# Kernel optimization log

Hardware: AMD Instinct MI355X
Metric: run time of the kernel (lower is better)

The kernel has to match this reference:

```python
import jax, jax.numpy as jnp
import numpy as np

N, E, B = 200000, 800000, 16
NODE_FEAT = 140  # last col = shape element type id
N_OPS, N_TYPES = 120, 8
OP_EMB, TYPE_EMB, CFG = 32, 4, 18
H = 64
CAT = (NODE_FEAT - 1) + TYPE_EMB + OP_EMB + CFG  # 193


def _lin(k, i, o):
    s = 1.0 / np.sqrt(i)
    return jax.random.uniform(k, (i, o), jnp.float32, -s, s)


def setup_inputs() -> dict:
    key = jax.random.key(0)
    ks = jax.random.split(key, 20)
    nf = jax.random.normal(ks[0], (N, NODE_FEAT - 1), jnp.float32)
    ty = jax.random.randint(ks[1], (N, 1), 0, N_TYPES).astype(jnp.float32)
    inp = {
        "node_feat": jnp.concatenate([nf, ty], axis=1),
        "node_config_feat": jax.random.normal(ks[2], (N, CFG), jnp.float32),
        "node_opcode": jax.random.randint(ks[3], (N,), 0, N_OPS),
        "edge_index": jax.random.randint(ks[4], (2, E), 0, N),
        "batch": jnp.sort(jax.random.randint(ks[5], (N,), 0, B)),
        "op_emb": jax.random.normal(ks[6], (N_OPS, OP_EMB), jnp.float32),
        "type_emb": jax.random.normal(ks[7], (N_TYPES, TYPE_EMB), jnp.float32),
        "lin_w": _lin(ks[8], CAT, 2 * H),
        "lin_b": jnp.zeros((2 * H,), jnp.float32),
        "post_w": _lin(ks[9], H, 1),
        "post_b": jnp.zeros((1,), jnp.float32),
    }
    kk = 10
    for l, ind in enumerate([2 * H, H, H]):
        inp[f"p{l}_wp"] = _lin(ks[kk], ind, ind); kk += 1  # SAGE project lin
        inp[f"p{l}_bp"] = jnp.zeros((ind,), jnp.float32)
        inp[f"p{l}_wl"] = _lin(ks[kk], ind, H); kk += 1    # lin_l (on aggregated)
        inp[f"p{l}_bl"] = jnp.zeros((H,), jnp.float32)
        inp[f"p{l}_wr"] = _lin(ks[kk], ind, H); kk += 1    # lin_r (root, no bias)
    return inp


def _sage(x, src, dst, deg_inv, wp, bp, wl, bl, wr):
    # PyG SAGEConv(project=True, normalize=True), mean aggregation
    xp = jax.nn.relu(x @ wp + bp)
    agg = jax.ops.segment_sum(xp[src], dst, num_segments=x.shape[0]) * deg_inv
    out = agg @ wl + bl + x @ wr
    n = jnp.linalg.norm(out, axis=-1, keepdims=True)
    return out / jnp.maximum(n, 1e-12)


def reference(node_feat, node_config_feat, node_opcode, edge_index, batch,
              op_emb, type_emb, lin_w, lin_b, post_w, post_b,
              p0_wp, p0_bp, p0_wl, p0_bl, p0_wr,
              p1_wp, p1_bp, p1_wl, p1_bl, p1_wr,
              p2_wp, p2_bp, p2_wl, p2_bl, p2_wr):
    lps = [(p0_wp, p0_bp, p0_wl, p0_bl, p0_wr),
           (p1_wp, p1_bp, p1_wl, p1_bl, p1_wr),
           (p2_wp, p2_bp, p2_wl, p2_bl, p2_wr)]
    ty = jnp.take(type_emb, node_feat[:, -1].astype(jnp.int32), axis=0)
    op = jnp.take(op_emb, node_opcode, axis=0)
    x = jnp.concatenate([node_feat[:, :-1], ty, op, node_config_feat], axis=-1)
    x = jax.nn.relu(x @ lin_w + lin_b)  # (N, 128)
    src, dst = edge_index[0], edge_index[1]
    deg = jax.ops.segment_sum(jnp.ones((E,), x.dtype), dst, num_segments=N)
    deg_inv = (1.0 / jnp.maximum(deg, 1.0))[:, None]
    for (wp, bp, wl, bl, wr) in lps:
        x = _sage(x, src, dst, deg_inv, wp, bp, wl, bl, wr)
    # global max + mean pool per graph
    gmax = jax.ops.segment_max(x, batch, num_segments=B)
    gsum = jax.ops.segment_sum(x, batch, num_segments=B)
    cnt = jax.ops.segment_sum(jnp.ones((N,), x.dtype), batch, num_segments=B)
    g = gmax + gsum / jnp.maximum(cnt, 1.0)[:, None]
    g = g / jnp.linalg.norm(g, axis=-1, keepdims=True)
    return g @ post_w + post_b  # (B, 1); eval path returns x_graph
```

## Files before the change

### kernel.cpp

```cpp
#include <hip/hip_runtime.h>

typedef _Float16 half8 __attribute__((ext_vector_type(8)));
typedef _Float16 h4 __attribute__((ext_vector_type(4)));
typedef float f32x4 __attribute__((ext_vector_type(4)));

__device__ __forceinline__ unsigned fkey(float f) {
  unsigned u = __float_as_uint(f);
  return (u & 0x80000000u) ? ~u : (u | 0x80000000u);
}
__device__ __forceinline__ float funkey(unsigned k) {
  unsigned u = (k & 0x80000000u) ? (k ^ 0x80000000u) : ~k;
  return __uint_as_float(u);
}

struct WD { const float* src; _Float16* dst; int K, NC, Kpad, base; };
struct WDs { WD d[10]; int total; };

__global__ __launch_bounds__(256) void k_wconv(WDs w) {
  int idx = blockIdx.x * 256 + threadIdx.x;
  if (idx >= w.total) return;
#pragma unroll
  for (int i = 0; i < 10; ++i) {
    int rel = idx - w.d[i].base;
    int sz = w.d[i].NC * w.d[i].Kpad;
    if (rel >= 0 && rel < sz) {
      int n = rel / w.d[i].Kpad;
      int k = rel - n * w.d[i].Kpad;
      w.d[i].dst[rel] = (k < w.d[i].K) ? (_Float16)w.d[i].src[(size_t)k * w.d[i].NC + n]
                                       : (_Float16)0.f;
      return;
    }
  }
}

__global__ __launch_bounds__(256) void k_count(const int* __restrict__ dst,
                                               int* __restrict__ counts, int E) {
  int e = blockIdx.x * 256 + threadIdx.x;
  if (e < E) atomicAdd(&counts[dst[e]], 1);
}

__global__ __launch_bounds__(256) void k_scan1(const int* __restrict__ counts,
                                               int* __restrict__ offsets,
                                               int* __restrict__ blockSums, int N) {
  __shared__ int sm[256];
  int tid = threadIdx.x;
  int gid = blockIdx.x * 256 + tid;
  int v = (gid < N) ? counts[gid] : 0;
  sm[tid] = v;
  __syncthreads();
  for (int off = 1; off < 256; off <<= 1) {
    int t = (tid >= off) ? sm[tid - off] : 0;
    __syncthreads();
    sm[tid] += t;
    __syncthreads();
  }
  if (gid < N) offsets[gid] = sm[tid] - v;
  if (tid == 255) blockSums[blockIdx.x] = sm[255];
}

__global__ __launch_bounds__(1024) void k_scan2(int* __restrict__ blockSums, int NB) {
  __shared__ int sm[1024];
  int tid = threadIdx.x;
  int v = (tid < NB) ? blockSums[tid] : 0;
  sm[tid] = v;
  __syncthreads();
  for (int off = 1; off < 1024; off <<= 1) {
    int t = (tid >= off) ? sm[tid - off] : 0;
    __syncthreads();
    sm[tid] += t;
    __syncthreads();
  }
  if (tid < NB) blockSums[tid] = sm[tid] - v;
}

__global__ __launch_bounds__(256) void k_scan3(const int* __restrict__ counts,
                                               int* __restrict__ offsets,
                                               const int* __restrict__ blockSums,
                                               int* __restrict__ fillpos,
                                               float* __restrict__ deginv, int N, int E) {
  int gid = blockIdx.x * 256 + threadIdx.x;
  if (gid < N) {
    int off = offsets[gid] + blockSums[gid >> 8];
    offsets[gid] = off;
    fillpos[gid] = off;
    deginv[gid] = 1.f / fmaxf((float)counts[gid], 1.f);
  }
  if (gid == 0) offsets[N] = E;
}

__global__ __launch_bounds__(256) void k_fill(const int* __restrict__ src,
                                              const int* __restrict__ dst,
                                              int* __restrict__ fillpos,
                                              int* __restrict__ esrc, int E) {
  int e = blockIdx.x * 256 + threadIdx.x;
  if (e < E) {
    int p = atomicAdd(&fillpos[dst[e]], 1);
    esrc[p] = src[e];
  }
}

__global__ __launch_bounds__(256) void k_feat(const float* __restrict__ node_feat,
                                              const float* __restrict__ cfgf,
                                              const int* __restrict__ opcode,
                                              const float* __restrict__ op_emb,
                                              const float* __restrict__ type_emb,
                                              _Float16* __restrict__ Out, int N) {
  __shared__ _Float16 sM[64 * 96];
  const int base = blockIdx.x * 64;

#pragma unroll
  for (int it = 0; it < 5; ++it) {
    int t = it * 256 + threadIdx.x;
    if (t >= 1088) break;
    int r = t / 17, c = t - r * 17;
    int n = base + r;
    if (n < N) {
      const float4* g = (const float4*)(node_feat + (size_t)n * 140 + c * 8);
      float4 v0 = g[0], v1 = g[1];
      half8 o;
      o[0] = (_Float16)v0.x; o[1] = (_Float16)v0.y;
      o[2] = (_Float16)v0.z; o[3] = (_Float16)v0.w;
      o[4] = (_Float16)v1.x; o[5] = (_Float16)v1.y;
      o[6] = (_Float16)v1.z; o[7] = (_Float16)v1.w;
      *(half8*)(Out + (size_t)n * 224 + c * 8) = o;
    }
  }

  const int wave = threadIdx.x >> 6, lane = threadIdx.x & 63;
#pragma unroll
  for (int it = 0; it < 3; ++it) {
    int cls = it * 4 + wave;
    if (cls >= 11) break;
    int r = lane, n = base + r;
    bool ok = (n < N);
    half8 o = half8{};
    if (cls == 0) {
      if (ok) {
        float4 v = *(const float4*)(node_feat + (size_t)n * 140 + 136);
        int ty = min(max((int)v.w, 0), 7);
        const float* te = type_emb + ty * 4;
        o[0] = (_Float16)v.x; o[1] = (_Float16)v.y; o[2] = (_Float16)v.z;
        o[3] = (_Float16)te[0]; o[4] = (_Float16)te[1];
        o[5] = (_Float16)te[2]; o[6] = (_Float16)te[3];
        o[7] = (_Float16)op_emb[opcode[n] * 32];
      }
    } else if (cls <= 3) {
      if (ok) {
        const float* oe = op_emb + opcode[n] * 32 + ((cls - 1) * 8 + 1);
#pragma unroll
        for (int j = 0; j < 8; ++j) o[j] = (_Float16)oe[j];
      }
    } else if (cls == 4) {
      if (ok) {
        const float* oe = op_emb + opcode[n] * 32;
#pragma unroll
        for (int j = 0; j < 7; ++j) o[j] = (_Float16)oe[25 + j];
        o[7] = (_Float16)cfgf[(size_t)n * 18];
      }
    } else if (cls <= 6) {
      if (ok) {
        const float* cf = cfgf + (size_t)n * 18 + ((cls - 5) * 8 + 1);
#pragma unroll
        for (int j = 0; j < 8; ++j) o[j] = (_Float16)cf[j];
      }
    } else if (cls == 7) {
      if (ok) o[0] = (_Float16)cfgf[(size_t)n * 18 + 17];
    }
    *(half8*)(sM + r * 96 + cls * 8) = o;
  }
  __syncthreads();

#pragma unroll
  for (int it = 0; it < 3; ++it) {
    int t = it * 256 + threadIdx.x;
    if (t >= 704) break;
    int r = t / 11, cc = t - r * 11;
    int n = base + r;
    if (n < N)
      *(half8*)(Out + (size_t)n * 224 + 136 + cc * 8) = *(const half8*)(sM + r * 96 + cc * 8);
  }
}

template <int K0, int K1, int NC, int MODE>
__global__ __launch_bounds__(256) void k_mm(
    const _Float16* __restrict__ A0, const _Float16* __restrict__ W0,
    const _Float16* __restrict__ A1, const _Float16* __restrict__ W1,
    const float* __restrict__ bias, _Float16* __restrict__ Out, int N) {
  constexpr int NT = NC / 16;
  constexpr int RT = 4;
  constexpr int KP0 = K0 + 8;
  constexpr int KP1 = K1 + 8;
  __shared__ _Float16 sB0[NC * KP0];
  __shared__ _Float16 sB1[(K1 > 0) ? (NC * KP1) : 8];

  for (int idx = threadIdx.x; idx < NC * (K0 / 8); idx += 256) {
    int nn = idx / (K0 / 8), k8 = idx - nn * (K0 / 8);
    *(half8*)(sB0 + nn * KP0 + k8 * 8) = *(const half8*)(W0 + (size_t)nn * K0 + k8 * 8);
  }
  if constexpr (K1 > 0) {
    for (int idx = threadIdx.x; idx < NC * (K1 / 8); idx += 256) {
      int nn = idx / (K1 / 8), k8 = idx - nn * (K1 / 8);
      *(half8*)(sB1 + nn * KP1 + k8 * 8) = *(const half8*)(W1 + (size_t)nn * K1 + k8 * 8);
    }
  }
  __syncthreads();

  const int lane = threadIdx.x & 63, wave = threadIdx.x >> 6;
  const int quad = lane >> 4, l15 = lane & 15;
  const int r0 = blockIdx.x * 256 + wave * 64;

  f32x4 acc[RT][NT];
#pragma unroll
  for (int rt = 0; rt < RT; ++rt)
#pragma unroll
    for (int t = 0; t < NT; ++t) acc[rt][t] = (f32x4)0.f;

  {
    const _Float16* ap = A0 + (size_t)(r0 + l15) * K0 + quad * 8;
#pragma unroll
    for (int k = 0; k < K0; k += 32) {
      half8 a[RT];
#pragma unroll
      for (int rt = 0; rt < RT; ++rt) a[rt] = *(const half8*)(ap + (size_t)rt * 16 * K0 + k);
#pragma unroll
      for (int t = 0; t < NT; ++t) {
        half8 b = *(const half8*)(sB0 + (t * 16 + l15) * KP0 + quad * 8 + k);
#pragma unroll
        for (int rt = 0; rt < RT; ++rt)
          acc[rt][t] = __builtin_amdgcn_mfma_f32_16x16x32_f16(a[rt], b, acc[rt][t], 0, 0, 0);
      }
    }
  }
  if constexpr (K1 > 0) {
    const _Float16* ap = A1 + (size_t)(r0 + l15) * K1 + quad * 8;
#pragma unroll
    for (int k = 0; k < K1; k += 32) {
      half8 a[RT];
#pragma unroll
      for (int rt = 0; rt < RT; ++rt) a[rt] = *(const half8*)(ap + (size_t)rt * 16 * K1 + k);
#pragma unroll
      for (int t = 0; t < NT; ++t) {
        half8 b = *(const half8*)(sB1 + (t * 16 + l15) * KP1 + quad * 8 + k);
#pragma unroll
        for (int rt = 0; rt < RT; ++rt)
          acc[rt][t] = __builtin_amdgcn_mfma_f32_16x16x32_f16(a[rt], b, acc[rt][t], 0, 0, 0);
      }
    }
  }

#pragma unroll
  for (int rt = 0; rt < RT; ++rt) {
#pragma unroll
    for (int t = 0; t < NT; ++t) {
      float bv = bias[t * 16 + l15];
      acc[rt][t][0] += bv; acc[rt][t][1] += bv;
      acc[rt][t][2] += bv; acc[rt][t][3] += bv;
    }
    if constexpr (MODE == 1) {
      f32x4 ss = (f32x4)0.f;
#pragma unroll
      for (int t = 0; t < NT; ++t) ss += acc[rt][t] * acc[rt][t];
#pragma unroll
      for (int j = 0; j < 4; ++j) {
        float s = ss[j];
        s += __shfl_xor(s, 1);
        s += __shfl_xor(s, 2);
        s += __shfl_xor(s, 4);
        s += __shfl_xor(s, 8);
        float sc = 1.f / fmaxf(sqrtf(s), 1e-12f);
#pragma unroll
        for (int t = 0; t < NT; ++t) acc[rt][t][j] *= sc;
      }
    } else {
#pragma unroll
      for (int t = 0; t < NT; ++t) {
        acc[rt][t][0] = fmaxf(acc[rt][t][0], 0.f);
        acc[rt][t][1] = fmaxf(acc[rt][t][1], 0.f);
        acc[rt][t][2] = fmaxf(acc[rt][t][2], 0.f);
        acc[rt][t][3] = fmaxf(acc[rt][t][3], 0.f);
      }
    }
#pragma unroll
    for (int j = 0; j < 4; ++j) {
      int r = r0 + rt * 16 + quad * 4 + j;
      if (r < N) {
#pragma unroll
        for (int t = 0; t < NT; ++t)
          Out[(size_t)r * NC + t * 16 + l15] = (_Float16)acc[rt][t][j];
      }
    }
  }
}

template <int NC>
__global__ __launch_bounds__(256) void k_agg(const _Float16* __restrict__ xp,
                                             const int* __restrict__ offs,
                                             const int* __restrict__ esrc,
                                             const float* __restrict__ deginv,
                                             _Float16* __restrict__ agg, int N) {
  constexpr int LPN = NC / 4;
  int t = blockIdx.x * 256 + threadIdx.x;
  int node = t / LPN;
  int lane = t - node * LPN;
  if (node >= N) return;
  int s0 = offs[node], s1 = offs[node + 1];
  double a0 = 0., a1 = 0., a2 = 0., a3 = 0.;
  for (int i = s0; i < s1; i += 4) {
    int nlast = s1 - 1;
    int e0 = esrc[i];
    int e1 = esrc[min(i + 1, nlast)];
    int e2 = esrc[min(i + 2, nlast)];
    int e3 = esrc[min(i + 3, nlast)];
    h4 v0 = ((const h4*)(xp + (size_t)e0 * NC))[lane];
    h4 v1 = ((const h4*)(xp + (size_t)e1 * NC))[lane];
    h4 v2 = ((const h4*)(xp + (size_t)e2 * NC))[lane];
    h4 v3 = ((const h4*)(xp + (size_t)e3 * NC))[lane];
    a0 += (double)(float)v0[0]; a1 += (double)(float)v0[1];
    a2 += (double)(float)v0[2]; a3 += (double)(float)v0[3];
    if (i + 1 < s1) { a0 += (double)(float)v1[0]; a1 += (double)(float)v1[1];
                      a2 += (double)(float)v1[2]; a3 += (double)(float)v1[3]; }
    if (i + 2 < s1) { a0 += (double)(float)v2[0]; a1 += (double)(float)v2[1];
                      a2 += (double)(float)v2[2]; a3 += (double)(float)v2[3]; }
    if (i + 3 < s1) { a0 += (double)(float)v3[0]; a1 += (double)(float)v3[1];
                      a2 += (double)(float)v3[2]; a3 += (double)(float)v3[3]; }
  }
  double di = (double)deginv[node];
  h4 o;
  o[0] = (_Float16)(a0 * di); o[1] = (_Float16)(a1 * di);
  o[2] = (_Float16)(a2 * di); o[3] = (_Float16)(a3 * di);
  ((h4*)(agg + (size_t)node * NC))[lane] = o;
}

__global__ __launch_bounds__(256) void k_pool1(const _Float16* __restrict__ x,
                                               const int* __restrict__ batch,
                                               unsigned* __restrict__ gkey,
                                               double* __restrict__ gsum,
                                               int* __restrict__ gcnt, int N) {
  int chunk = blockIdx.x * 4 + (threadIdx.x >> 6);
  int lane = threadIdx.x & 63;
  int n0 = chunk * 64;
  if (n0 >= N) return;
  int n1 = min(n0 + 64, N);
  float rmax = -3.4e38f;
  double rsum = 0.;
  int rcnt = 0, curb = batch[n0];
  for (int n = n0; n < n1; ++n) {
    int b = batch[n];
    if (b != curb) {
      atomicMax(&gkey[curb * 64 + lane], fkey(rmax));
      atomicAdd(&gsum[curb * 64 + lane], rsum);
      if (lane == 0) atomicAdd(&gcnt[curb], rcnt);
      rmax = -3.4e38f; rsum = 0.; rcnt = 0; curb = b;
    }
    float v = (float)x[(size_t)n * 64 + lane];
    rmax = fmaxf(rmax, v);
    rsum += (double)v;
    rcnt++;
  }
  atomicMax(&gkey[curb * 64 + lane], fkey(rmax));
  atomicAdd(&gsum[curb * 64 + lane], rsum);
  if (lane == 0) atomicAdd(&gcnt[curb], rcnt);
}

__global__ __launch_bounds__(1024) void k_pool2(const unsigned* __restrict__ gkey,
                                                const double* __restrict__ gsum,
                                                const int* __restrict__ gcnt,
                                                const float* __restrict__ post_w,
                                                const float* __restrict__ post_b,
                                                float* __restrict__ out) {
  int b = threadIdx.x >> 6, lane = threadIdx.x & 63;
  float m = funkey(gkey[b * 64 + lane]);
  double s = gsum[b * 64 + lane];
  double c = (double)gcnt[b];
  float g = m + (float)(s / fmax(c, 1.0));
  float ss = g * g;
#pragma unroll
  for (int off = 1; off < 64; off <<= 1) ss += __shfl_xor(ss, off);
  float gn = g / fmaxf(sqrtf(ss), 1e-30f);
  float contrib = gn * post_w[lane];
#pragma unroll
  for (int off = 1; off < 64; off <<= 1) contrib += __shfl_xor(contrib, off);
  if (lane == 0) out[b] = contrib + post_b[0];
}

extern "C" void kernel_launch(void* const* d_in, const int* in_sizes, int n_in,
                              void* d_out, int out_size, void* d_ws, size_t ws_size,
                              hipStream_t stream) {
  const float* node_feat = (const float*)d_in[0];
  const float* cfgf      = (const float*)d_in[1];
  const int*   opcode    = (const int*)d_in[2];
  const int*   eidx      = (const int*)d_in[3];
  const int*   batch     = (const int*)d_in[4];
  const float* op_emb    = (const float*)d_in[5];
  const float* type_emb  = (const float*)d_in[6];
  const float* lin_w     = (const float*)d_in[7];
  const float* lin_b     = (const float*)d_in[8];
  const float* post_w    = (const float*)d_in[9];
  const float* post_b    = (const float*)d_in[10];
  const float* wp[3] = {(const float*)d_in[11], (const float*)d_in[16], (const float*)d_in[21]};
  const float* bp[3] = {(const float*)d_in[12], (const float*)d_in[17], (const float*)d_in[22]};
  const float* wl[3] = {(const float*)d_in[13], (const float*)d_in[18], (const float*)d_in[23]};
  const float* bl[3] = {(const float*)d_in[14], (const float*)d_in[19], (const float*)d_in[24]};
  const float* wr[3] = {(const float*)d_in[15], (const float*)d_in[20], (const float*)d_in[25]};

  const int N = in_sizes[2];
  const int E = in_sizes[3] / 2;
  const int NPAD = ((N + 255) / 256) * 256;
  const int* e_src = eidx;
  const int* e_dst = eidx + E;

  char* p = (char*)d_ws;
  auto alloc = [&](size_t bytes) -> void* {
    void* r = (void*)p;
    p += (bytes + 255) & ~(size_t)255;
    return r;
  };
  _Float16* F  = (_Float16*)alloc((size_t)NPAD * 224 * 2);
  _Float16* X1 = (_Float16*)alloc((size_t)NPAD * 128 * 2);
  _Float16* R2 = (_Float16*)alloc((size_t)NPAD * 128 * 2);
  _Float16* R3 = (_Float16*)alloc((size_t)NPAD * 128 * 2);
  _Float16* WT = (_Float16*)alloc(86016 * 2);
  int* counts    = (int*)alloc((size_t)N * 4);
  int* offsets   = (int*)alloc((size_t)(N + 1) * 4);
  int* fillpos   = (int*)alloc((size_t)N * 4);
  float* deginv  = (float*)alloc((size_t)N * 4);
  int* blockSums = (int*)alloc(1024 * 4);
  int* esrc      = (int*)alloc((size_t)E * 4);
  unsigned* gkey = (unsigned*)alloc(16 * 64 * 4);
  double* gsum   = (double*)alloc(16 * 64 * 8);
  int* gcnt      = (int*)alloc(16 * 4);
  (void)ws_size; (void)n_in; (void)out_size;

  _Float16* WTenc = WT + 0;
  _Float16* WTp0  = WT + 28672;
  _Float16* WTl0  = WT + 45056;
  _Float16* WTr0  = WT + 53248;
  _Float16* WTp1  = WT + 61440;
  _Float16* WTl1  = WT + 65536;
  _Float16* WTr1  = WT + 69632;
  _Float16* WTp2  = WT + 73728;
  _Float16* WTl2  = WT + 77824;
  _Float16* WTr2  = WT + 81920;

  WDs wds;
  wds.d[0] = {lin_w, WTenc, 193, 128, 224, 0};
  wds.d[1] = {wp[0], WTp0, 128, 128, 128, 28672};
  wds.d[2] = {wl[0], WTl0, 128, 64, 128, 45056};
  wds.d[3] = {wr[0], WTr0, 128, 64, 128, 53248};
  wds.d[4] = {wp[1], WTp1, 64, 64, 64, 61440};
  wds.d[5] = {wl[1], WTl1, 64, 64, 64, 65536};
  wds.d[6] = {wr[1], WTr1, 64, 64, 64, 69632};
  wds.d[7] = {wp[2], WTp2, 64, 64, 64, 73728};
  wds.d[8] = {wl[2], WTl2, 64, 64, 64, 77824};
  wds.d[9] = {wr[2], WTr2, 64, 64, 64, 81920};
  wds.total = 86016;

  hipMemsetAsync(counts, 0, (size_t)N * 4, stream);
  hipMemsetAsync(gkey, 0, 16 * 64 * 4, stream);
  hipMemsetAsync(gsum, 0, 16 * 64 * 8, stream);
  hipMemsetAsync(gcnt, 0, 16 * 4, stream);

  const int nbE = (E + 255) / 256;
  const int nbN = (N + 255) / 256;
  const int nbMM = NPAD / 256;
  const int nbA128 = ((size_t)N * 32 + 255) / 256;
  const int nbA64  = ((size_t)N * 16 + 255) / 256;
  const int nbP = ((N + 63) / 64 + 3) / 4;

  k_wconv<<<(86016 + 255) / 256, 256, 0, stream>>>(wds);
  k_count<<<nbE, 256, 0, stream>>>(e_dst, counts, E);
  k_scan1<<<nbN, 256, 0, stream>>>(counts, offsets, blockSums, N);
  k_scan2<<<1, 1024, 0, stream>>>(blockSums, nbN);
  k_scan3<<<nbN, 256, 0, stream>>>(counts, offsets, blockSums, fillpos, deginv, N, E);
  k_fill<<<nbE, 256, 0, stream>>>(e_src, e_dst, fillpos, esrc, E);

  k_feat<<<(N + 63) / 64, 256, 0, stream>>>(node_feat, cfgf, opcode, op_emb, type_emb, F, N);
  k_mm<224, 0, 128, 0><<<nbMM, 256, 0, stream>>>(F, WTenc, nullptr, nullptr, lin_b, X1, N);

  k_mm<128, 0, 128, 0><<<nbMM, 256, 0, stream>>>(X1, WTp0, nullptr, nullptr, bp[0], R2, N);
  k_agg<128><<<nbA128, 256, 0, stream>>>(R2, offsets, esrc, deginv, R3, N);
  k_mm<128, 128, 64, 1><<<nbMM, 256, 0, stream>>>(R3, WTl0, X1, WTr0, bl[0], R2, N);
  k_mm<64, 0, 64, 0><<<nbMM, 256, 0, stream>>>(R2, WTp1, nullptr, nullptr, bp[1], R3, N);
  k_agg<64><<<nbA64, 256, 0, stream>>>(R3, offsets, esrc, deginv, X1, N);
  k_mm<64, 64, 64, 1><<<nbMM, 256, 0, stream>>>(X1, WTl1, R2, WTr1, bl[1], R3, N);
  k_mm<64, 0, 64, 0><<<nbMM, 256, 0, stream>>>(R3, WTp2, nullptr, nullptr, bp[2], X1, N);
  k_agg<64><<<nbA64, 256, 0, stream>>>(X1, offsets, esrc, deginv, R2, N);
  k_mm<64, 64, 64, 1><<<nbMM, 256, 0, stream>>>(R2, WTl2, R3, WTr2, bl[2], X1, N);

  k_pool1<<<nbP, 256, 0, stream>>>(X1, batch, gkey, gsum, gcnt, N);
  k_pool2<<<1, 1024, 0, stream>>>(gkey, gsum, gcnt, post_w, post_b, (float*)d_out);
}
```

Baseline: 733.1 us.

## Reorder layer-0 SAGE to project before aggregation, shrinking gather width to 64

Layer 0 now applies the lin_l weights (128→64) to the projected features before mean aggregation, using linearity of the mean. The edge gather therefore reads 64-wide rows instead of 128-wide. The aggregated result is then added through an identity-weight second operand in the fused matmul. An extra matmul pass with a new MODE 2 (no activation, no bias) is added, and the node_feat conversion loop in k_feat is restructured to issue all loads before the conversions and stores. Applying lin_l before aggregation changes the fp16 rounding order, and the identity matmul adds some wasted MFMA work.

```diff
diff --git a/kernel.cpp b/kernel.cpp
--- a/kernel.cpp
+++ b/kernel.cpp
@@ -31,6 +31,11 @@
       return;
     }
   }
+}
+
+__global__ __launch_bounds__(256) void k_ident(_Float16* __restrict__ w) {
+  int i = blockIdx.x * 256 + threadIdx.x;
+  if (i < 4096) w[i] = (_Float16)(((i >> 6) == (i & 63)) ? 1.f : 0.f);
 }
 
 __global__ __launch_bounds__(256) void k_count(const int* __restrict__ dst,
@@ -108,21 +113,32 @@
   __shared__ _Float16 sM[64 * 96];
   const int base = blockIdx.x * 64;
 
-#pragma unroll
-  for (int it = 0; it < 5; ++it) {
-    int t = it * 256 + threadIdx.x;
-    if (t >= 1088) break;
-    int r = t / 17, c = t - r * 17;
-    int n = base + r;
-    if (n < N) {
-      const float4* g = (const float4*)(node_feat + (size_t)n * 140 + c * 8);
-      float4 v0 = g[0], v1 = g[1];
-      half8 o;
-      o[0] = (_Float16)v0.x; o[1] = (_Float16)v0.y;
-      o[2] = (_Float16)v0.z; o[3] = (_Float16)v0.w;
-      o[4] = (_Float16)v1.x; o[5] = (_Float16)v1.y;
-      o[6] = (_Float16)v1.z; o[7] = (_Float16)v1.w;
-      *(half8*)(Out + (size_t)n * 224 + c * 8) = o;
+  {
+    float4 va[5], vb[5];
+    int rr[5], cc[5];
+    bool ok[5];
+#pragma unroll
+    for (int it = 0; it < 5; ++it) {
+      int t = it * 256 + threadIdx.x;
+      int r = t / 17, c = t - r * 17;
+      rr[it] = r; cc[it] = c;
+      ok[it] = (t < 1088) && (base + r < N);
+      if (ok[it]) {
+        const float4* g = (const float4*)(node_feat + (size_t)(base + r) * 140 + c * 8);
+        va[it] = g[0];
+        vb[it] = g[1];
+      }
+    }
+#pragma unroll
+    for (int it = 0; it < 5; ++it) {
+      if (ok[it]) {
+        half8 o;
+        o[0] = (_Float16)va[it].x; o[1] = (_Float16)va[it].y;
+        o[2] = (_Float16)va[it].z; o[3] = (_Float16)va[it].w;
+        o[4] = (_Float16)vb[it].x; o[5] = (_Float16)vb[it].y;
+        o[6] = (_Float16)vb[it].z; o[7] = (_Float16)vb[it].w;
+        *(half8*)(Out + (size_t)(base + rr[it]) * 224 + cc[it] * 8) = o;
+      }
     }
   }
 
@@ -250,11 +266,13 @@
 
 #pragma unroll
   for (int rt = 0; rt < RT; ++rt) {
-#pragma unroll
-    for (int t = 0; t < NT; ++t) {
-      float bv = bias[t * 16 + l15];
-      acc[rt][t][0] += bv; acc[rt][t][1] += bv;
-      acc[rt][t][2] += bv; acc[rt][t][3] += bv;
+    if (bias != nullptr) {
+#pragma unroll
+      for (int t = 0; t < NT; ++t) {
+        float bv = bias[t * 16 + l15];
+        acc[rt][t][0] += bv; acc[rt][t][1] += bv;
+        acc[rt][t][2] += bv; acc[rt][t][3] += bv;
+      }
     }
     if constexpr (MODE == 1) {
       f32x4 ss = (f32x4)0.f;
@@ -271,7 +289,7 @@
 #pragma unroll
         for (int t = 0; t < NT; ++t) acc[rt][t][j] *= sc;
       }
-    } else {
+    } else if constexpr (MODE == 0) {
 #pragma unroll
       for (int t = 0; t < NT; ++t) {
         acc[rt][t][0] = fmaxf(acc[rt][t][0], 0.f);
@@ -419,7 +437,7 @@
   _Float16* X1 = (_Float16*)alloc((size_t)NPAD * 128 * 2);
   _Float16* R2 = (_Float16*)alloc((size_t)NPAD * 128 * 2);
   _Float16* R3 = (_Float16*)alloc((size_t)NPAD * 128 * 2);
-  _Float16* WT = (_Float16*)alloc(86016 * 2);
+  _Float16* WT = (_Float16*)alloc(90112 * 2);
   int* counts    = (int*)alloc((size_t)N * 4);
   int* offsets   = (int*)alloc((size_t)(N + 1) * 4);
   int* fillpos   = (int*)alloc((size_t)N * 4);
@@ -441,6 +459,7 @@
   _Float16* WTp2  = WT + 73728;
   _Float16* WTl2  = WT + 77824;
   _Float16* WTr2  = WT + 81920;
+  _Float16* WTid  = WT + 86016;
 
   WDs wds;
   wds.d[0] = {lin_w, WTenc, 193, 128, 224, 0};
@@ -463,11 +482,11 @@
   const int nbE = (E + 255) / 256;
   const int nbN = (N + 255) / 256;
   const int nbMM = NPAD / 256;
-  const int nbA128 = ((size_t)N * 32 + 255) / 256;
-  const int nbA64  = ((size_t)N * 16 + 255) / 256;
+  const int nbA64 = ((size_t)N * 16 + 255) / 256;
   const int nbP = ((N + 63) / 64 + 3) / 4;
 
   k_wconv<<<(86016 + 255) / 256, 256, 0, stream>>>(wds);
+  k_ident<<<16, 256, 0, stream>>>(WTid);
   k_count<<<nbE, 256, 0, stream>>>(e_dst, counts, E);
   k_scan1<<<nbN, 256, 0, stream>>>(counts, offsets, blockSums, N);
   k_scan2<<<1, 1024, 0, stream>>>(blockSums, nbN);
@@ -478,15 +497,16 @@
   k_mm<224, 0, 128, 0><<<nbMM, 256, 0, stream>>>(F, WTenc, nullptr, nullptr, lin_b, X1, N);
 
   k_mm<128, 0, 128, 0><<<nbMM, 256, 0, stream>>>(X1, WTp0, nullptr, nullptr, bp[0], R2, N);
-  k_agg<128><<<nbA128, 256, 0, stream>>>(R2, offsets, esrc, deginv, R3, N);
-  k_mm<128, 128, 64, 1><<<nbMM, 256, 0, stream>>>(R3, WTl0, X1, WTr0, bl[0], R2, N);
-  k_mm<64, 0, 64, 0><<<nbMM, 256, 0, stream>>>(R2, WTp1, nullptr, nullptr, bp[1], R3, N);
+  k_mm<128, 0, 64, 2><<<nbMM, 256, 0, stream>>>(R2, WTl0, nullptr, nullptr, nullptr, R3, N);
+  k_agg<64><<<nbA64, 256, 0, stream>>>(R3, offsets, esrc, deginv, R2, N);
+  k_mm<128, 64, 64, 1><<<nbMM, 256, 0, stream>>>(X1, WTr0, R2, WTid, bl[0], R3, N);
+  k_mm<64, 0, 64, 0><<<nbMM, 256, 0, stream>>>(R3, WTp1, nullptr, nullptr, bp[1], R2, N);
+  k_agg<64><<<nbA64, 256, 0, stream>>>(R2, offsets, esrc, deginv, X1, N);
+  k_mm<64, 64, 64, 1><<<nbMM, 256, 0, stream>>>(X1, WTl1, R3, WTr1, bl[1], R2, N);
+  k_mm<64, 0, 64, 0><<<nbMM, 256, 0, stream>>>(R2, WTp2, nullptr, nullptr, bp[2], R3, N);
   k_agg<64><<<nbA64, 256, 0, stream>>>(R3, offsets, esrc, deginv, X1, N);
-  k_mm<64, 64, 64, 1><<<nbMM, 256, 0, stream>>>(X1, WTl1, R2, WTr1, bl[1], R3, N);
-  k_mm<64, 0, 64, 0><<<nbMM, 256, 0, stream>>>(R3, WTp2, nullptr, nullptr, bp[2], X1, N);
-  k_agg<64><<<nbA64, 256, 0, stream>>>(X1, offsets, esrc, deginv, R2, N);
-  k_mm<64, 64, 64, 1><<<nbMM, 256, 0, stream>>>(R2, WTl2, R3, WTr2, bl[2], X1, N);
-
-  k_pool1<<<nbP, 256, 0, stream>>>(X1, batch, gkey, gsum, gcnt, N);
+  k_mm<64, 64, 64, 1><<<nbMM, 256, 0, stream>>>(X1, WTl2, R2, WTr2, bl[2], R3, N);
+
+  k_pool1<<<nbP, 256, 0, stream>>>(R3, batch, gkey, gsum, gcnt, N);
   k_pool2<<<1, 1024, 0, stream>>>(gkey, gsum, gcnt, post_w, post_b, (float*)d_out);
 }
```

New measurement: 750.4 us. +2.4%, slower.
